# Kernel tuning notes

Measured on AMD Instinct MI355X. Metric: run time of the kernel, lower is better.

The kernel has to match this reference:

```python
import jax, jax.numpy as jnp
import numpy as np

B, G, D = 8192, 32, 64
N_USERS, N_ITEMS, N_GROUPS = 200000, 50000, 20000
CLS_BIAS = 0.5


def setup_inputs() -> dict:
    key = jax.random.key(0)
    ks = jax.random.split(key, 16)
    s = lambda k, shape: (jax.random.normal(k, shape, dtype=jnp.float32) * 0.05)
    return {
        'group_inputs': jax.random.randint(ks[0], (B,), 0, N_GROUPS),
        'item_inputs': jax.random.randint(ks[1], (B,), 0, N_ITEMS),
        'members': jax.random.randint(ks[2], (B, G), 0, N_USERS),
        'user_table': s(ks[3], (N_USERS, D)),
        'item_table': s(ks[4], (N_ITEMS, D)),
        'group_table': s(ks[5], (N_GROUPS, D)),
        'group_embedds': s(ks[6], (N_GROUPS, D)),
        'att_w1': s(ks[7], (2 * D, 16)), 'att_b1': jnp.zeros((16,), jnp.float32),
        'att_w2': s(ks[8], (16, 1)), 'att_b2': jnp.zeros((1,), jnp.float32),
        'cls_w': s(ks[9], (1, 2)), 'cls_b': jnp.zeros((2,), jnp.float32),
        'pred_w1': s(ks[10], (3 * D, 8)), 'pred_b1': jnp.zeros((8,), jnp.float32),
        'pred_w2': s(ks[11], (8, 1)), 'pred_b2': jnp.zeros((1,), jnp.float32),
    }


def reference(group_inputs, item_inputs, members, user_table, item_table,
              group_table, group_embedds, att_w1, att_b1, att_w2, att_b2,
              cls_w, cls_b, pred_w1, pred_b1, pred_w2, pred_b2):
    # gather member / item embeddings (irregular access hot path)
    mem_emb = user_table[members]                      # [B, G, D]
    item_emb = item_table[item_inputs]                 # [B, D]
    gi = jnp.concatenate(
        [mem_emb, jnp.broadcast_to(item_emb[:, None, :], mem_emb.shape)], axis=-1)  # [B, G, 2D]
    # AttentionLayer(2D): Linear -> ReLU -> Linear(->1) -> softmax over members
    h = jax.nn.relu(jnp.einsum('bgc,ch->bgh', gi, att_w1) + att_b1)
    scores = (jnp.einsum('bgh,ho->bgo', h, att_w2) + att_b2)[..., 0]  # [B, G]
    at_wt = jax.nn.softmax(scores, axis=-1)            # [B, G]
    # routing branch: classifier on the max attention weight
    max_idx = jnp.argmax(at_wt, axis=-1)               # [B]
    max_w = jnp.max(at_wt, axis=-1, keepdims=True)     # [B, 1]
    cls_scores = max_w @ cls_w + cls_b                 # [B, 2]
    cls_scores = cls_scores.at[:, 1].add(CLS_BIAS)
    pred_cls = jnp.argmax(jax.nn.softmax(cls_scores, axis=-1), axis=-1)  # [B]
    leader_emb = jnp.take_along_axis(mem_emb, max_idx[:, None, None], axis=1)[:, 0]  # [B, D]
    weighted_emb = jnp.einsum('bg,bgd->bd', at_wt, mem_emb)
    g_att = jnp.where((pred_cls == 1)[:, None], leader_emb, weighted_emb)
    # pure group embedding + precomputed group embeds
    g_pure = group_table[group_inputs] + group_embedds[group_inputs]
    g = g_att + g_pure                                 # [B, D]
    # PredictLayer(3D): Linear -> ReLU -> Linear -> sigmoid
    elem = g * item_emb
    new_embeds = jnp.concatenate([elem, g, item_emb], axis=-1)  # [B, 3D]
    ph = jax.nn.relu(new_embeds @ pred_w1 + pred_b1)
    y = jax.nn.sigmoid(ph @ pred_w2 + pred_b2)         # [B, 1]
    return new_embeds, y, at_wt, pred_cls
```

## Files before the change

### kernel.cpp

```cpp
#include <hip/hip_runtime.h>

#define BB 8192
#define GG 32
#define DD 64

__global__ __launch_bounds__(64, 4)
void hhgr_kernel(const int* __restrict__ group_inputs,
                 const int* __restrict__ item_inputs,
                 const int* __restrict__ members,
                 const float* __restrict__ user_table,
                 const float* __restrict__ item_table,
                 const float* __restrict__ group_table,
                 const float* __restrict__ group_embedds,
                 const float* __restrict__ att_w1, const float* __restrict__ att_b1,
                 const float* __restrict__ att_w2, const float* __restrict__ att_b2,
                 const float* __restrict__ cls_w, const float* __restrict__ cls_b,
                 const float* __restrict__ pred_w1, const float* __restrict__ pred_b1,
                 const float* __restrict__ pred_w2, const float* __restrict__ pred_b2,
                 float* __restrict__ out)
{
    __shared__ float smem[2176 + 64 + 32 + 32];
    float* mem_lds   = smem;
    float* item_lds  = smem + 2176;
    float* score_lds = smem + 2240;
    float* awt_lds   = smem + 2272;
    float* ne_lds    = smem;

    const int b    = blockIdx.x;
    const int lane = threadIdx.x;
    const int o    = lane & 15;
    const int q    = lane >> 4;
    const int h2   = q & 1;
    const int gg   = q >> 1;

    const int gidx = group_inputs[b];
    const int iidx = item_inputs[b];
    const int midx = members[b * GG + (lane & 31)];

    const float it = item_table[(size_t)iidx * DD + lane];
    item_lds[lane] = it;

#pragma unroll
    for (int i = 0; i < 8; ++i) {
        const int r   = 4 * i + q;
        const int row = __shfl(midx, r);
        const float4 v = *(const float4*)(user_table + (size_t)row * DD + o * 4);
        *(float4*)(mem_lds + r * 68 + o * 4) = v;
    }

    float wl[32];
#pragma unroll
    for (int j = 0; j < 32; ++j)
        wl[j] = att_w1[(h2 * 32 + j) * 16 + o];
    const float w2v = att_w2[o];
    const float b2  = att_b2[0];

    __syncthreads();

    float hiacc = 0.f;
#pragma unroll
    for (int k2 = 0; k2 < 16; ++k2) {
        const int k = q * 16 + k2;
        hiacc = fmaf(item_lds[k], att_w1[(64 + k) * 16 + o], hiacc);
    }
    hiacc += __shfl_xor(hiacc, 16);
    hiacc += __shfl_xor(hiacc, 32);
    const float hib = hiacc + att_b1[o];

    for (int gb = 0; gb < 16; ++gb) {
        const int g = gb * 2 + gg;
        const float* mrow = mem_lds + g * 68 + h2 * 32;
        float acc = 0.f;
#pragma unroll
        for (int i = 0; i < 8; ++i) {
            const float4 m4 = *(const float4*)(mrow + i * 4);
            acc = fmaf(m4.x, wl[i * 4 + 0], acc);
            acc = fmaf(m4.y, wl[i * 4 + 1], acc);
            acc = fmaf(m4.z, wl[i * 4 + 2], acc);
            acc = fmaf(m4.w, wl[i * 4 + 3], acc);
        }
        acc += __shfl_xor(acc, 16);
        const float h = fmaxf(acc + hib, 0.f);
        float c = h * w2v;
        c += __shfl_xor(c, 1);
        c += __shfl_xor(c, 2);
        c += __shfl_xor(c, 4);
        c += __shfl_xor(c, 8);
        if ((lane & 31) == 0) score_lds[g] = c + b2;
    }
    __syncthreads();

    const int gl = lane & 31;
    const float s = score_lds[gl];
    float m = s;
#pragma unroll
    for (int mk = 1; mk <= 16; mk <<= 1) m = fmaxf(m, __shfl_xor(m, mk));
    const float e = expf(s - m);
    float sum = e;
#pragma unroll
    for (int mk = 1; mk <= 16; mk <<= 1) sum += __shfl_xor(sum, mk);
    const float w = e / sum;
    if (lane < 32) {
        awt_lds[lane] = w;
        out[(size_t)BB * 193 + (size_t)b * GG + lane] = w;
    }
    float wmax = w;
#pragma unroll
    for (int mk = 1; mk <= 16; mk <<= 1) wmax = fmaxf(wmax, __shfl_xor(wmax, mk));
    int idxc = (w == wmax) ? gl : 1000;
#pragma unroll
    for (int mk = 1; mk <= 16; mk <<= 1) idxc = min(idxc, __shfl_xor(idxc, mk));

    const float cs0 = wmax * cls_w[0] + cls_b[0];
    const float cs1 = (wmax * cls_w[1] + cls_b[1]) + 0.5f;
    const int pred  = (cs1 > cs0) ? 1 : 0;

    __syncthreads();

    float gatt;
    if (pred == 1) {
        gatt = mem_lds[idxc * 68 + lane];
    } else {
        float acc = 0.f;
        for (int g = 0; g < GG; ++g)
            acc = fmaf(awt_lds[g], mem_lds[g * 68 + lane], acc);
        gatt = acc;
    }
    const float gp = group_table[(size_t)gidx * DD + lane]
                   + group_embedds[(size_t)gidx * DD + lane];
    const float gv = gatt + gp;
    const float el = gv * it;

    out[(size_t)b * 192 + lane]       = el;
    out[(size_t)b * 192 + 64 + lane]  = gv;
    out[(size_t)b * 192 + 128 + lane] = it;

    __syncthreads();
    ne_lds[lane]        = el;
    ne_lds[64 + lane]   = gv;
    ne_lds[128 + lane]  = it;
    __syncthreads();

    const int j  = lane & 7;
    const int sg = lane >> 3;
    float pacc = 0.f;
#pragma unroll
    for (int cc = 0; cc < 24; ++cc) {
        const int c = sg * 24 + cc;
        pacc = fmaf(ne_lds[c], pred_w1[c * 8 + j], pacc);
    }
    pacc += __shfl_xor(pacc, 8);
    pacc += __shfl_xor(pacc, 16);
    pacc += __shfl_xor(pacc, 32);
    const float ph = fmaxf(pacc + pred_b1[j], 0.f);
    float t = ph * pred_w2[j];
    t += __shfl_xor(t, 1);
    t += __shfl_xor(t, 2);
    t += __shfl_xor(t, 4);
    const float yv = 1.f / (1.f + expf(-(t + pred_b2[0])));

    if (lane == 0) {
        out[(size_t)BB * 192 + b] = yv;
        out[(size_t)BB * 225 + b] = (float)pred;
    }
}

extern "C" void kernel_launch(void* const* d_in, const int* in_sizes, int n_in,
                              void* d_out, int out_size, void* d_ws, size_t ws_size,
                              hipStream_t stream) {
    const int*   group_inputs = (const int*)d_in[0];
    const int*   item_inputs  = (const int*)d_in[1];
    const int*   members      = (const int*)d_in[2];
    const float* user_table   = (const float*)d_in[3];
    const float* item_table   = (const float*)d_in[4];
    const float* group_table  = (const float*)d_in[5];
    const float* group_embedds= (const float*)d_in[6];
    const float* att_w1 = (const float*)d_in[7];
    const float* att_b1 = (const float*)d_in[8];
    const float* att_w2 = (const float*)d_in[9];
    const float* att_b2 = (const float*)d_in[10];
    const float* cls_w  = (const float*)d_in[11];
    const float* cls_b  = (const float*)d_in[12];
    const float* pred_w1 = (const float*)d_in[13];
    const float* pred_b1 = (const float*)d_in[14];
    const float* pred_w2 = (const float*)d_in[15];
    const float* pred_b2 = (const float*)d_in[16];
    float* out = (float*)d_out;

    hipLaunchKernelGGL(hhgr_kernel, dim3(BB), dim3(64), 0, stream,
                       group_inputs, item_inputs, members, user_table, item_table,
                       group_table, group_embedds, att_w1, att_b1, att_w2, att_b2,
                       cls_w, cls_b, pred_w1, pred_b1, pred_w2, pred_b2, out);
}
```

Measured before the change: 150.8 us.

## Remap to one lane per member with eight batch rows per block

Each 32-lane half-wave now handles one batch row, and each lane owns one group member. A lane loads its full user embedding into registers and computes its attention hidden layer against broadcast weights, so the LDS staging and most block barriers go away. Cross-lane reductions use DPP row operations plus one shuffle. The weighted-sum and leader paths re-read user rows from global memory, which relies on caches rather than LDS. Register pressure rises (64 floats of embedding plus 16 accumulators per lane), and the per-lane row loads are less coalesced.

```diff
diff --git a/kernel.cpp b/kernel.cpp
--- a/kernel.cpp
+++ b/kernel.cpp
@@ -4,7 +4,46 @@
 #define GG 32
 #define DD 64
 
-__global__ __launch_bounds__(64, 4)
+#define QUAD_XOR1 0xB1
+#define QUAD_XOR2 0x4E
+#define ROW_ROR4  0x124
+#define ROW_ROR8  0x128
+
+template<int CTRL>
+__device__ __forceinline__ float dpp_mov(float x) {
+    return __int_as_float(__builtin_amdgcn_update_dpp(
+        __float_as_int(x), __float_as_int(x), CTRL, 0xF, 0xF, false));
+}
+__device__ __forceinline__ float row16_sum(float x) {
+    x += dpp_mov<QUAD_XOR1>(x);
+    x += dpp_mov<QUAD_XOR2>(x);
+    x += dpp_mov<ROW_ROR4>(x);
+    x += dpp_mov<ROW_ROR8>(x);
+    return x;
+}
+__device__ __forceinline__ float row16_max(float x) {
+    x = fmaxf(x, dpp_mov<QUAD_XOR1>(x));
+    x = fmaxf(x, dpp_mov<QUAD_XOR2>(x));
+    x = fmaxf(x, dpp_mov<ROW_ROR4>(x));
+    x = fmaxf(x, dpp_mov<ROW_ROR8>(x));
+    return x;
+}
+template<int CTRL>
+__device__ __forceinline__ int dpp_mov_i(int x) {
+    return __builtin_amdgcn_update_dpp(x, x, CTRL, 0xF, 0xF, false);
+}
+__device__ __forceinline__ int row16_min_i(int x) {
+    x = min(x, dpp_mov_i<QUAD_XOR1>(x));
+    x = min(x, dpp_mov_i<QUAD_XOR2>(x));
+    x = min(x, dpp_mov_i<ROW_ROR4>(x));
+    x = min(x, dpp_mov_i<ROW_ROR8>(x));
+    return x;
+}
+__device__ __forceinline__ float half_sum(float x) { x = row16_sum(x); return x + __shfl_xor(x, 16); }
+__device__ __forceinline__ float half_max(float x) { x = row16_max(x); return fmaxf(x, __shfl_xor(x, 16)); }
+__device__ __forceinline__ int   half_min_i(int x) { x = row16_min_i(x); return min(x, __shfl_xor(x, 16)); }
+
+__global__ __launch_bounds__(256)
 void hhgr_kernel(const int* __restrict__ group_inputs,
                  const int* __restrict__ item_inputs,
                  const int* __restrict__ members,
@@ -19,147 +58,141 @@
                  const float* __restrict__ pred_w2, const float* __restrict__ pred_b2,
                  float* __restrict__ out)
 {
-    __shared__ float smem[2176 + 64 + 32 + 32];
-    float* mem_lds   = smem;
-    float* item_lds  = smem + 2176;
-    float* score_lds = smem + 2240;
-    float* awt_lds   = smem + 2272;
-    float* ne_lds    = smem;
-
-    const int b    = blockIdx.x;
-    const int lane = threadIdx.x;
-    const int o    = lane & 15;
-    const int q    = lane >> 4;
-    const int h2   = q & 1;
-    const int gg   = q >> 1;
-
+    __shared__ float awt_s[8][32];
+    __shared__ int   midx_s[8][32];
+
+    const int tid  = threadIdx.x;
+    const int m    = tid & 31;
+    const int slot = tid >> 5;
+    const int wl   = tid & 63;
+    const int hw   = wl >> 5;
+    const int b    = blockIdx.x * 8 + slot;
+
+    const int midx = members[b * GG + m];
+    const int iidx = item_inputs[b];
     const int gidx = group_inputs[b];
-    const int iidx = item_inputs[b];
-    const int midx = members[b * GG + (lane & 31)];
-
-    const float it = item_table[(size_t)iidx * DD + lane];
-    item_lds[lane] = it;
-
-#pragma unroll
-    for (int i = 0; i < 8; ++i) {
-        const int r   = 4 * i + q;
-        const int row = __shfl(midx, r);
-        const float4 v = *(const float4*)(user_table + (size_t)row * DD + o * 4);
-        *(float4*)(mem_lds + r * 68 + o * 4) = v;
-    }
-
-    float wl[32];
-#pragma unroll
-    for (int j = 0; j < 32; ++j)
-        wl[j] = att_w1[(h2 * 32 + j) * 16 + o];
-    const float w2v = att_w2[o];
-    const float b2  = att_b2[0];
-
-    __syncthreads();
-
-    float hiacc = 0.f;
-#pragma unroll
-    for (int k2 = 0; k2 < 16; ++k2) {
-        const int k = q * 16 + k2;
-        hiacc = fmaf(item_lds[k], att_w1[(64 + k) * 16 + o], hiacc);
-    }
-    hiacc += __shfl_xor(hiacc, 16);
-    hiacc += __shfl_xor(hiacc, 32);
-    const float hib = hiacc + att_b1[o];
-
-    for (int gb = 0; gb < 16; ++gb) {
-        const int g = gb * 2 + gg;
-        const float* mrow = mem_lds + g * 68 + h2 * 32;
-        float acc = 0.f;
-#pragma unroll
-        for (int i = 0; i < 8; ++i) {
-            const float4 m4 = *(const float4*)(mrow + i * 4);
-            acc = fmaf(m4.x, wl[i * 4 + 0], acc);
-            acc = fmaf(m4.y, wl[i * 4 + 1], acc);
-            acc = fmaf(m4.z, wl[i * 4 + 2], acc);
-            acc = fmaf(m4.w, wl[i * 4 + 3], acc);
-        }
-        acc += __shfl_xor(acc, 16);
-        const float h = fmaxf(acc + hib, 0.f);
-        float c = h * w2v;
-        c += __shfl_xor(c, 1);
-        c += __shfl_xor(c, 2);
-        c += __shfl_xor(c, 4);
-        c += __shfl_xor(c, 8);
-        if ((lane & 31) == 0) score_lds[g] = c + b2;
-    }
-    __syncthreads();
-
-    const int gl = lane & 31;
-    const float s = score_lds[gl];
-    float m = s;
-#pragma unroll
-    for (int mk = 1; mk <= 16; mk <<= 1) m = fmaxf(m, __shfl_xor(m, mk));
-    const float e = expf(s - m);
-    float sum = e;
-#pragma unroll
-    for (int mk = 1; mk <= 16; mk <<= 1) sum += __shfl_xor(sum, mk);
-    const float w = e / sum;
-    if (lane < 32) {
-        awt_lds[lane] = w;
-        out[(size_t)BB * 193 + (size_t)b * GG + lane] = w;
-    }
-    float wmax = w;
-#pragma unroll
-    for (int mk = 1; mk <= 16; mk <<= 1) wmax = fmaxf(wmax, __shfl_xor(wmax, mk));
-    int idxc = (w == wmax) ? gl : 1000;
-#pragma unroll
-    for (int mk = 1; mk <= 16; mk <<= 1) idxc = min(idxc, __shfl_xor(idxc, mk));
-
-    const float cs0 = wmax * cls_w[0] + cls_b[0];
-    const float cs1 = (wmax * cls_w[1] + cls_b[1]) + 0.5f;
+
+    float4 mr[16];
+    {
+        const float4* urow = (const float4*)(user_table + (size_t)midx * DD);
+#pragma unroll
+        for (int i = 0; i < 16; ++i) mr[i] = urow[i];
+    }
+
+    float h[16];
+    {
+        const float2 it2 = *(const float2*)(item_table + (size_t)iidx * DD + 2 * m);
+        const float4* wa = (const float4*)(att_w1 + (64 + 2 * m) * 16);
+        const float4* wb = (const float4*)(att_w1 + (65 + 2 * m) * 16);
+#pragma unroll
+        for (int q4 = 0; q4 < 4; ++q4) {
+            const float4 a  = wa[q4];
+            const float4 bq = wb[q4];
+            h[4 * q4 + 0] = fmaf(it2.y, bq.x, it2.x * a.x);
+            h[4 * q4 + 1] = fmaf(it2.y, bq.y, it2.x * a.y);
+            h[4 * q4 + 2] = fmaf(it2.y, bq.z, it2.x * a.z);
+            h[4 * q4 + 3] = fmaf(it2.y, bq.w, it2.x * a.w);
+        }
+#pragma unroll
+        for (int i = 0; i < 16; ++i)
+            h[i] = half_sum(h[i]) + att_b1[i];
+    }
+
+#pragma unroll
+    for (int i = 0; i < 16; ++i) {
+#pragma unroll
+        for (int j = 0; j < 4; ++j) {
+            const float mk = (j == 0) ? mr[i].x : (j == 1) ? mr[i].y
+                           : (j == 2) ? mr[i].z : mr[i].w;
+            const float* wr = att_w1 + (4 * i + j) * 16;
+#pragma unroll
+            for (int oo = 0; oo < 16; ++oo)
+                h[oo] = fmaf(mk, wr[oo], h[oo]);
+        }
+    }
+
+    float sc = att_b2[0];
+#pragma unroll
+    for (int oo = 0; oo < 16; ++oo)
+        sc = fmaf(fmaxf(h[oo], 0.f), att_w2[oo], sc);
+
+    const float smax = half_max(sc);
+    const float e    = expf(sc - smax);
+    const float ssum = half_sum(e);
+    const float w    = e / ssum;
+    out[(size_t)BB * 193 + (size_t)b * GG + m] = w;
+
+    const float wmax = half_max(w);
+    const int   idx  = half_min_i((w == wmax) ? m : 1000);
+
+    const float cs0 = fmaf(wmax, cls_w[0], cls_b[0]);
+    const float cs1 = fmaf(wmax, cls_w[1], cls_b[1]) + 0.5f;
     const int pred  = (cs1 > cs0) ? 1 : 0;
 
-    __syncthreads();
-
-    float gatt;
-    if (pred == 1) {
-        gatt = mem_lds[idxc * 68 + lane];
+    float gA, gB;
+    if (pred) {
+        const int lmidx = __shfl(midx, hw * 32 + idx);
+        const float* lrow = user_table + (size_t)lmidx * DD;
+        gA = lrow[m];
+        gB = lrow[m + 32];
     } else {
-        float acc = 0.f;
-        for (int g = 0; g < GG; ++g)
-            acc = fmaf(awt_lds[g], mem_lds[g * 68 + lane], acc);
-        gatt = acc;
-    }
-    const float gp = group_table[(size_t)gidx * DD + lane]
-                   + group_embedds[(size_t)gidx * DD + lane];
-    const float gv = gatt + gp;
-    const float el = gv * it;
-
-    out[(size_t)b * 192 + lane]       = el;
-    out[(size_t)b * 192 + 64 + lane]  = gv;
-    out[(size_t)b * 192 + 128 + lane] = it;
-
-    __syncthreads();
-    ne_lds[lane]        = el;
-    ne_lds[64 + lane]   = gv;
-    ne_lds[128 + lane]  = it;
-    __syncthreads();
-
-    const int j  = lane & 7;
-    const int sg = lane >> 3;
-    float pacc = 0.f;
-#pragma unroll
-    for (int cc = 0; cc < 24; ++cc) {
-        const int c = sg * 24 + cc;
-        pacc = fmaf(ne_lds[c], pred_w1[c * 8 + j], pacc);
-    }
-    pacc += __shfl_xor(pacc, 8);
-    pacc += __shfl_xor(pacc, 16);
-    pacc += __shfl_xor(pacc, 32);
-    const float ph = fmaxf(pacc + pred_b1[j], 0.f);
-    float t = ph * pred_w2[j];
-    t += __shfl_xor(t, 1);
-    t += __shfl_xor(t, 2);
-    t += __shfl_xor(t, 4);
-    const float yv = 1.f / (1.f + expf(-(t + pred_b2[0])));
-
-    if (lane == 0) {
+        awt_s[slot][m]  = w;
+        midx_s[slot][m] = midx;
+        __builtin_amdgcn_s_waitcnt(0);
+        float accA = 0.f, accB = 0.f;
+        for (int g = 0; g < GG; ++g) {
+            const float wg = awt_s[slot][g];
+            const float* grow = user_table + (size_t)midx_s[slot][g] * DD;
+            accA = fmaf(wg, grow[m], accA);
+            accB = fmaf(wg, grow[m + 32], accB);
+        }
+        gA = accA; gB = accB;
+    }
+
+    const float gpA = group_table[(size_t)gidx * DD + m]      + group_embedds[(size_t)gidx * DD + m];
+    const float gpB = group_table[(size_t)gidx * DD + m + 32] + group_embedds[(size_t)gidx * DD + m + 32];
+    const float itA = item_table[(size_t)iidx * DD + m];
+    const float itB = item_table[(size_t)iidx * DD + m + 32];
+    const float gvA = gA + gpA, gvB = gB + gpB;
+    const float elA = gvA * itA, elB = gvB * itB;
+
+    const size_t nb = (size_t)b * 192;
+    out[nb + m]        = elA;  out[nb + 32 + m]  = elB;
+    out[nb + 64 + m]   = gvA;  out[nb + 96 + m]  = gvB;
+    out[nb + 128 + m]  = itA;  out[nb + 160 + m] = itB;
+
+    float p8[8];
+#pragma unroll
+    for (int j = 0; j < 8; ++j) p8[j] = 0.f;
+
+    {
+        const float vals[6] = { elA, elB, gvA, gvB, itA, itB };
+        const int   cols[6] = { m, m + 32, 64 + m, 96 + m, 128 + m, 160 + m };
+#pragma unroll
+        for (int t = 0; t < 6; ++t) {
+            const float4* wr = (const float4*)(pred_w1 + cols[t] * 8);
+            const float4 w0 = wr[0], w1v = wr[1];
+            p8[0] = fmaf(vals[t], w0.x, p8[0]);
+            p8[1] = fmaf(vals[t], w0.y, p8[1]);
+            p8[2] = fmaf(vals[t], w0.z, p8[2]);
+            p8[3] = fmaf(vals[t], w0.w, p8[3]);
+            p8[4] = fmaf(vals[t], w1v.x, p8[4]);
+            p8[5] = fmaf(vals[t], w1v.y, p8[5]);
+            p8[6] = fmaf(vals[t], w1v.z, p8[6]);
+            p8[7] = fmaf(vals[t], w1v.w, p8[7]);
+        }
+    }
+#pragma unroll
+    for (int j = 0; j < 8; ++j)
+        p8[j] = half_sum(p8[j]) + pred_b1[j];
+
+    float t2 = pred_b2[0];
+#pragma unroll
+    for (int j = 0; j < 8; ++j)
+        t2 = fmaf(fmaxf(p8[j], 0.f), pred_w2[j], t2);
+    const float yv = 1.f / (1.f + expf(-t2));
+
+    if (m == 0) {
         out[(size_t)BB * 192 + b] = yv;
         out[(size_t)BB * 225 + b] = (float)pred;
     }
@@ -168,26 +201,26 @@
 extern "C" void kernel_launch(void* const* d_in, const int* in_sizes, int n_in,
                               void* d_out, int out_size, void* d_ws, size_t ws_size,
                               hipStream_t stream) {
-    const int*   group_inputs = (const int*)d_in[0];
-    const int*   item_inputs  = (const int*)d_in[1];
-    const int*   members      = (const int*)d_in[2];
-    const float* user_table   = (const float*)d_in[3];
-    const float* item_table   = (const float*)d_in[4];
-    const float* group_table  = (const float*)d_in[5];
-    const float* group_embedds= (const float*)d_in[6];
-    const float* att_w1 = (const float*)d_in[7];
-    const float* att_b1 = (const float*)d_in[8];
-    const float* att_w2 = (const float*)d_in[9];
-    const float* att_b2 = (const float*)d_in[10];
-    const float* cls_w  = (const float*)d_in[11];
-    const float* cls_b  = (const float*)d_in[12];
+    const int*   group_inputs  = (const int*)d_in[0];
+    const int*   item_inputs   = (const int*)d_in[1];
+    const int*   members       = (const int*)d_in[2];
+    const float* user_table    = (const float*)d_in[3];
+    const float* item_table    = (const float*)d_in[4];
+    const float* group_table   = (const float*)d_in[5];
+    const float* group_embedds = (const float*)d_in[6];
+    const float* att_w1  = (const float*)d_in[7];
+    const float* att_b1  = (const float*)d_in[8];
+    const float* att_w2  = (const float*)d_in[9];
+    const float* att_b2  = (const float*)d_in[10];
+    const float* cls_w   = (const float*)d_in[11];
+    const float* cls_b   = (const float*)d_in[12];
     const float* pred_w1 = (const float*)d_in[13];
     const float* pred_b1 = (const float*)d_in[14];
     const float* pred_w2 = (const float*)d_in[15];
     const float* pred_b2 = (const float*)d_in[16];
     float* out = (float*)d_out;
 
-    hipLaunchKernelGGL(hhgr_kernel, dim3(BB), dim3(64), 0, stream,
+    hipLaunchKernelGGL(hhgr_kernel, dim3(BB / 8), dim3(256), 0, stream,
                        group_inputs, item_inputs, members, user_table, item_table,
                        group_table, group_embedds, att_w1, att_b1, att_w2, att_b2,
                        cls_w, cls_b, pred_w1, pred_b1, pred_w2, pred_b2, out);
```

After: 144.8 us. 3.9% less time.
